# Kernel tuning notes

Hardware: AMD Instinct MI355X
Metric: run time of the kernel (lower is better)

The kernel has to match this reference:

```python
import jax, jax.numpy as jnp
import numpy as np

N, S, E, H = 2, 2048, 1024, 16
D = E // H  # head_dim = 64


def setup_inputs() -> dict:
    key = jax.random.key(0)
    k1, k2, k3 = jax.random.split(key, 3)
    x = jax.random.normal(k1, (N, S, E), dtype=jnp.float32)
    # Xavier-uniform-scaled weights (torch Linear layout: [out_features, in_features])
    lim_qkv = (6.0 / (E + 3 * E)) ** 0.5
    qkv_w = jax.random.uniform(k2, (3 * E, E), dtype=jnp.float32, minval=-lim_qkv, maxval=lim_qkv)
    lim_o = (6.0 / (E + E)) ** 0.5
    o_w = jax.random.uniform(k3, (E, E), dtype=jnp.float32, minval=-lim_o, maxval=lim_o)
    # causal look-ahead mask: positions where mask == 0 are excluded
    attn_mask = jnp.tril(jnp.ones((S, S), dtype=jnp.int32))
    return {"x": x, "attn_mask": attn_mask, "qkv_w": qkv_w, "o_w": o_w}


def reference(x, attn_mask, qkv_w, o_w):
    n, s, e = x.shape
    qkv = x @ qkv_w.T                              # (N, S, 3E)
    q, k, v = jnp.split(qkv, 3, axis=-1)
    # (N, S, E) -> (N, H, S, D)
    def to_heads(t):
        return t.reshape(n, s, H, D).transpose(0, 2, 1, 3)
    q, k, v = to_heads(q), to_heads(k), to_heads(v)
    scale = 1.0 / jnp.sqrt(jnp.asarray(D, dtype=x.dtype))
    logits = jnp.einsum('bhqd,bhkd->bhqk', q, k) * scale   # (N, H, S, S)
    mask = attn_mask.reshape(1, 1, s, s)                    # expand_mask: 2D -> (1,1,S,S)
    logits = jnp.where(mask == 0, -jnp.inf, logits)
    attn_weights = jax.nn.softmax(logits, axis=-1)
    values = jnp.einsum('bhqk,bhkd->bhqd', attn_weights, v)  # (N, H, S, D)
    values = values.transpose(0, 2, 1, 3).reshape(n, s, e)
    o = values @ o_w.T
    return o
```

## Files before the change

### kernel.cpp

```cpp
#include <hip/hip_runtime.h>
#include <math.h>

typedef unsigned short u16;
typedef unsigned int uint;
typedef __attribute__((ext_vector_type(8))) short bf16x8;
typedef __attribute__((ext_vector_type(8))) _Float16 half8;
typedef __attribute__((ext_vector_type(4))) float floatx4;

__device__ __forceinline__ u16 f2bf(float f) {
  union { float f; uint u; } c; c.f = f;
  return (u16)((c.u + 0x7FFFu + ((c.u >> 16) & 1u)) >> 16);
}
__device__ __forceinline__ float bf2f(u16 h) {
  union { uint u; float f; } c; c.u = ((uint)h) << 16;
  return c.f;
}
__device__ __forceinline__ u16 h2u(_Float16 h) {
  union { _Float16 h; u16 u; } c; c.h = h;
  return c.u;
}

#if __has_builtin(__builtin_amdgcn_exp2f)
#define EX2 __builtin_amdgcn_exp2f
#else
#define EX2 exp2f
#endif

__device__ __forceinline__ void gl_lds16(const u16* g, u16* l) {
  __builtin_amdgcn_global_load_lds(
      (const __attribute__((address_space(1))) uint*)g,
      (__attribute__((address_space(3))) uint*)l, 16, 0, 0);
}

__device__ __forceinline__ void store_c(u16* p, float v) { *p = f2bf(v); }
__device__ __forceinline__ void store_c(float* p, float v) { *p = v; }

#define ROR16(x, n)                                                        \
  __builtin_bit_cast(float, __builtin_amdgcn_update_dpp(                   \
      __builtin_bit_cast(int, (x)), __builtin_bit_cast(int, (x)),          \
      0x120 + (n), 0xF, 0xF, false))
__device__ __forceinline__ float rsum16(float x) {
  x += ROR16(x, 8); x += ROR16(x, 4); x += ROR16(x, 2); x += ROR16(x, 1);
  return x;
}

__global__ __launch_bounds__(256) void cvt_all(const float* __restrict__ x,
                                               const float* __restrict__ qw,
                                               const float* __restrict__ ow,
                                               u16* __restrict__ xb,
                                               u16* __restrict__ wb,
                                               u16* __restrict__ ob) {
  int bx = blockIdx.x;
  const float* src; u16* dst; int off;
  if (bx < 2048) { src = x; dst = xb; off = bx; }
  else if (bx < 3584) { src = qw; dst = wb; off = bx - 2048; }
  else { src = ow; dst = ob; off = bx - 3584; }
  int i = (off * 256 + threadIdx.x) * 8;
  float4 a = *(const float4*)(src + i);
  float4 b = *(const float4*)(src + i + 4);
  bf16x8 r;
  r[0] = (short)f2bf(a.x); r[1] = (short)f2bf(a.y);
  r[2] = (short)f2bf(a.z); r[3] = (short)f2bf(a.w);
  r[4] = (short)f2bf(b.x); r[5] = (short)f2bf(b.y);
  r[6] = (short)f2bf(b.z); r[7] = (short)f2bf(b.w);
  *(bf16x8*)(dst + i) = r;
}

__global__ __launch_bounds__(256) void vtrans(const u16* __restrict__ qkv,
                                              u16* __restrict__ vt) {
  constexpr int S = 2048, E = 1024, TE = 3072;
  __shared__ u16 tile[64 * 72];
  const int t = threadIdx.x;
  const int kv0 = blockIdx.x * 64;
  const int bh = blockIdx.y, b = bh >> 4, h = bh & 15;
  const u16* src = qkv + (size_t)b * S * TE + 2 * E + h * 64;
#pragma unroll
  for (int i = 0; i < 2; ++i) {
    int c = t + i * 256;
    int kv = c >> 3, d0 = (c & 7) * 8;
    *(bf16x8*)&tile[kv * 72 + d0] = *(const bf16x8*)&src[(size_t)(kv0 + kv) * TE + d0];
  }
  __syncthreads();
  u16* dst = vt + (size_t)bh * 64 * S + kv0;
#pragma unroll
  for (int i = 0; i < 2; ++i) {
    int c = t + i * 256;
    int d = c >> 3, k0 = (c & 7) * 8;
    bf16x8 r;
#pragma unroll
    for (int j = 0; j < 8; ++j)
      r[j] = (short)h2u((_Float16)bf2f(tile[(k0 + j) * 72 + d]));
    *(bf16x8*)&dst[(size_t)d * S + k0] = r;
  }
}

template <typename TC>
__global__ __launch_bounds__(256) void gemm_bt(const u16* __restrict__ A,
                                               const u16* __restrict__ B,
                                               TC* __restrict__ C,
                                               int K, int N) {
  __shared__ __align__(16) u16 lds_a[128 * 64];
  __shared__ __align__(16) u16 lds_b[128 * 64];
  const int t = threadIdx.x;
  const int w = t >> 6, lane = t & 63, quad = lane >> 4, lr = lane & 15;
  const int wr = w >> 1, wc = w & 1;
  const int m0 = blockIdx.y * 128, n0 = blockIdx.x * 128;

  const int srow = lane >> 3;
  const int scol = ((lane & 7) ^ srow) * 8;
  const u16* Ab = A + (size_t)(m0 + w * 32 + srow) * K + scol;
  const u16* Bb = B + (size_t)(n0 + w * 32 + srow) * K + scol;
  u16* la = lds_a + (w * 32) * 64;
  u16* lb = lds_b + (w * 32) * 64;

  floatx4 acc[4][4];
#pragma unroll
  for (int i = 0; i < 4; ++i)
#pragma unroll
    for (int j = 0; j < 4; ++j) acc[i][j] = {0.f, 0.f, 0.f, 0.f};

  for (int k0 = 0; k0 < K; k0 += 64) {
#pragma unroll
    for (int j = 0; j < 4; ++j) {
      gl_lds16(Ab + (size_t)(j * 8) * K + k0, la + j * 8 * 64);
      gl_lds16(Bb + (size_t)(j * 8) * K + k0, lb + j * 8 * 64);
    }
    __syncthreads();
#pragma unroll
    for (int kk = 0; kk < 2; ++kk) {
      bf16x8 af[4], bfr[4];
#pragma unroll
      for (int mi = 0; mi < 4; ++mi)
        af[mi] = *(const bf16x8*)&lds_a[(wr * 64 + mi * 16 + lr) * 64 +
                                        (((kk * 4 + quad) ^ (lr & 7)) * 8)];
#pragma unroll
      for (int ni = 0; ni < 4; ++ni)
        bfr[ni] = *(const bf16x8*)&lds_b[(wc * 64 + ni * 16 + lr) * 64 +
                                         (((kk * 4 + quad) ^ (lr & 7)) * 8)];
#pragma unroll
      for (int mi = 0; mi < 4; ++mi)
#pragma unroll
        for (int ni = 0; ni < 4; ++ni)
          acc[mi][ni] = __builtin_amdgcn_mfma_f32_16x16x32_bf16(
              af[mi], bfr[ni], acc[mi][ni], 0, 0, 0);
    }
    __syncthreads();
  }
#pragma unroll
  for (int mi = 0; mi < 4; ++mi)
#pragma unroll
    for (int r = 0; r < 4; ++r) {
      int m = m0 + wr * 64 + mi * 16 + quad * 4 + r;
#pragma unroll
      for (int ni = 0; ni < 4; ++ni) {
        int n = n0 + wc * 64 + ni * 16 + lr;
        store_c(&C[(size_t)m * N + n], acc[mi][ni][r]);
      }
    }
}

__global__ __launch_bounds__(256) void attn_fwd(const u16* __restrict__ qkv,
                                                const u16* __restrict__ vt,
                                                u16* __restrict__ out) {
  constexpr int S = 2048, E = 1024, TE = 3072;
  constexpr float NEG = -1e30f;
  __shared__ __align__(16) u16 lds_k[2][128 * 64];
  __shared__ __align__(16) u16 lds_vt[2][64 * 128];
  __shared__ __align__(16) u16 lds_p[64 * 128];
  const int t = threadIdx.x;
  const int w = t >> 6, lane = t & 63, quad = lane >> 4, lr = lane & 15;
  const int lin = (int)blockIdx.x;
  const int xcd = lin & 7, j = lin >> 3;
  const int bh = xcd + 8 * (j & 3);
  const int bx = j >> 2;
  const int b = bh >> 4, h = bh & 15;
  const size_t base = (size_t)b * S * TE;
  const u16* kbase = qkv + base + E + h * 64;
  const u16* vtb = vt + (size_t)bh * 64 * S;

  const int srow = lane >> 3;
  const int scol = ((lane & 7) ^ srow) * 8;
  const int vrow = lane >> 4;

  for (int ph = 0; ph < 2; ++ph) {
    const int qt = ph ? (31 - bx) : bx;
    const int q0 = qt * 64;
    const int nkt = (qt + 2) >> 1;

    const float QS = 0.125f * 1.44269504f;
    bf16x8 qf[2];
#pragma unroll
    for (int kk = 0; kk < 2; ++kk) {
      bf16x8 q = *(const bf16x8*)&qkv[base + (size_t)(q0 + w * 16 + lr) * TE +
                                      h * 64 + kk * 32 + quad * 8];
#pragma unroll
      for (int jj = 0; jj < 8; ++jj) q[jj] = (short)f2bf(bf2f((u16)q[jj]) * QS);
      qf[kk] = q;
    }

    float lst[4];
    floatx4 oacc[4];
#pragma unroll
    for (int r = 0; r < 4; ++r) lst[r] = 0.f;
#pragma unroll
    for (int di = 0; di < 4; ++di) oacc[di] = {0.f, 0.f, 0.f, 0.f};

    __syncthreads();

#pragma unroll
    for (int i = 0; i < 4; ++i) {
      int r0 = w * 8 + i * 32;
      gl_lds16(kbase + (size_t)(r0 + srow) * TE + scol, &lds_k[0][r0 * 64]);
    }
#pragma unroll
    for (int i = 0; i < 4; ++i) {
      int d0 = w * 4 + i * 16;
      int d = d0 + vrow;
      int cbg = ((lane & 15) ^ (d & 15)) * 8;
      gl_lds16(vtb + (size_t)d * S + cbg, &lds_vt[0][d0 * 128]);
    }

    for (int kt = 0; kt < nkt; ++kt) {
      const int bi = kt & 1;
      __syncthreads();
      if (kt + 1 < nkt) {
        const int bn = bi ^ 1;
#pragma unroll
        for (int i = 0; i < 4; ++i) {
          int r0 = w * 8 + i * 32;
          gl_lds16(kbase + (size_t)(128 * (kt + 1) + r0 + srow) * TE + scol,
                   &lds_k[bn][r0 * 64]);
        }
#pragma unroll
        for (int i = 0; i < 4; ++i) {
          int d0 = w * 4 + i * 16;
          int d = d0 + vrow;
          int cbg = ((lane & 15) ^ (d & 15)) * 8;
          gl_lds16(vtb + (size_t)d * S + 128 * (kt + 1) + cbg,
                   &lds_vt[bn][d0 * 128]);
        }
      }

      floatx4 st[8];
#pragma unroll
      for (int ni = 0; ni < 8; ++ni) st[ni] = {-4.f, -4.f, -4.f, -4.f};
#pragma unroll
      for (int kk = 0; kk < 2; ++kk) {
        bf16x8 kb[8];
#pragma unroll
        for (int ni = 0; ni < 8; ++ni)
          kb[ni] = *(const bf16x8*)&lds_k[bi][(ni * 16 + lr) * 64 +
                                             (((kk * 4 + quad) ^ (lr & 7)) * 8)];
#pragma unroll
        for (int ni = 0; ni < 8; ++ni)
          st[ni] = __builtin_amdgcn_mfma_f32_16x16x32_bf16(qf[kk], kb[ni], st[ni], 0, 0, 0);
      }

      const bool diag = (kt == nkt - 1);
      const int doff = (qt & 1) ? 64 : 0;
#pragma unroll
      for (int r = 0; r < 4; ++r) {
        const int rl = w * 16 + quad * 4 + r;
        if (diag) {
          const int thr = rl + doff;
#pragma unroll
          for (int ni = 0; ni < 8; ++ni)
            if (ni * 16 + lr > thr) st[ni][r] = NEG;
        }
        float pv[8];
#pragma unroll
        for (int ni = 0; ni < 8; ++ni) pv[ni] = EX2(st[ni][r]);
        lst[r] += ((pv[0] + pv[1]) + (pv[2] + pv[3])) +
                  ((pv[4] + pv[5]) + (pv[6] + pv[7]));
        const int swr = rl & 15;
#pragma unroll
        for (int ni = 0; ni < 8; ++ni) {
          int cb = (ni << 1) + (lr >> 3);
          lds_p[rl * 128 + (((cb ^ swr) << 3) + (lr & 7))] = h2u((_Float16)pv[ni]);
        }
      }

#pragma unroll
      for (int kk = 0; kk < 4; ++kk) {
        const int rl2 = w * 16 + lr;
        half8 pf = *(const half8*)&lds_p[rl2 * 128 + ((((kk << 2) + quad) ^ lr) << 3)];
        half8 vb[4];
#pragma unroll
        for (int di = 0; di < 4; ++di)
          vb[di] = *(const half8*)&lds_vt[bi][(di * 16 + lr) * 128 +
                                              ((((kk << 2) + quad) ^ lr) << 3)];
#pragma unroll
        for (int di = 0; di < 4; ++di)
          oacc[di] = __builtin_amdgcn_mfma_f32_16x16x32_f16(pf, vb[di], oacc[di], 0, 0, 0);
      }
    }

#pragma unroll
    for (int r = 0; r < 4; ++r) {
      int sg = q0 + w * 16 + quad * 4 + r;
      float inv_l = 1.f / rsum16(lst[r]);
#pragma unroll
      for (int di = 0; di < 4; ++di)
        out[((size_t)(b * S + sg)) * E + h * 64 + di * 16 + lr] =
            f2bf(oacc[di][r] * inv_l);
    }
  }
}

extern "C" void kernel_launch(void* const* d_in, const int* in_sizes, int n_in,
                              void* d_out, int out_size, void* d_ws, size_t ws_size,
                              hipStream_t stream) {
  constexpr int NB = 2, S = 2048, E = 1024;
  constexpr int M = NB * S;
  const float* x = (const float*)d_in[0];
  const float* qkv_w = (const float*)d_in[2];
  const float* o_w = (const float*)d_in[3];
  float* out = (float*)d_out;

  u16* qkv = (u16*)d_ws;
  u16* vt = qkv + (size_t)M * 3 * E;
  u16* xb = vt + (size_t)32 * 64 * S;
  u16* attn_o = xb;
  u16* wb = xb + (size_t)M * E;
  u16* ob = wb + (size_t)3 * E * E;

  cvt_all<<<4096, 256, 0, stream>>>(x, qkv_w, o_w, xb, wb, ob);
  gemm_bt<u16><<<dim3(3 * E / 128, M / 128), 256, 0, stream>>>(xb, wb, qkv, E, 3 * E);
  vtrans<<<dim3(S / 64, NB * 16), 256, 0, stream>>>(qkv, vt);
  attn_fwd<<<512, 256, 0, stream>>>(qkv, vt, attn_o);
  gemm_bt<float><<<dim3(E / 128, M / 128), 256, 0, stream>>>(attn_o, ob, out, E, E);
}
```

Before: 187.5 us.

## Enlarge attention query tile to 128 rows and add 64-row output GEMM

Attention blocks now each process 128 query rows, with each wave handling two 16-row groups, so every K/V tile loaded into shared memory is reused twice as much. K rows are loaded in a permuted order so that each lane's S values land contiguously, which lets the P tile be written to a per-wave buffer with vector stores. V fragments are hoisted out of the row-group loop. The grid is halved to 256 blocks with launch_bounds(256,1). The output projection switches to a 64x128-tile GEMM that launches more blocks. Register pressure grows and the grid may underfill the CUs.

```diff
diff --git a/kernel.cpp b/kernel.cpp
--- a/kernel.cpp
+++ b/kernel.cpp
@@ -159,58 +159,129 @@
     }
 }
 
-__global__ __launch_bounds__(256) void attn_fwd(const u16* __restrict__ qkv,
-                                                const u16* __restrict__ vt,
-                                                u16* __restrict__ out) {
+template <typename TC>
+__global__ __launch_bounds__(256) void gemm_bt64(const u16* __restrict__ A,
+                                                 const u16* __restrict__ B,
+                                                 TC* __restrict__ C,
+                                                 int K, int N) {
+  __shared__ __align__(16) u16 lds_a[64 * 64];
+  __shared__ __align__(16) u16 lds_b[128 * 64];
+  const int t = threadIdx.x;
+  const int w = t >> 6, lane = t & 63, quad = lane >> 4, lr = lane & 15;
+  const int m0 = blockIdx.y * 64, n0 = blockIdx.x * 128;
+
+  const int srow = lane >> 3;
+  const int scol = ((lane & 7) ^ srow) * 8;
+  const u16* Ab = A + (size_t)(m0 + srow) * K + scol;
+  const u16* Bb = B + (size_t)(n0 + srow) * K + scol;
+
+  floatx4 acc[4][2];
+#pragma unroll
+  for (int i = 0; i < 4; ++i)
+#pragma unroll
+    for (int j = 0; j < 2; ++j) acc[i][j] = {0.f, 0.f, 0.f, 0.f};
+
+  for (int k0 = 0; k0 < K; k0 += 64) {
+#pragma unroll
+    for (int i = 0; i < 2; ++i)
+      gl_lds16(Ab + (size_t)((w * 2 + i) * 8) * K + k0, &lds_a[(w * 2 + i) * 8 * 64]);
+#pragma unroll
+    for (int i = 0; i < 4; ++i)
+      gl_lds16(Bb + (size_t)((w * 4 + i) * 8) * K + k0, &lds_b[(w * 4 + i) * 8 * 64]);
+    __syncthreads();
+#pragma unroll
+    for (int kk = 0; kk < 2; ++kk) {
+      bf16x8 af[4], bfr[2];
+#pragma unroll
+      for (int mi = 0; mi < 4; ++mi)
+        af[mi] = *(const bf16x8*)&lds_a[(mi * 16 + lr) * 64 +
+                                        (((kk * 4 + quad) ^ (lr & 7)) * 8)];
+#pragma unroll
+      for (int ni = 0; ni < 2; ++ni)
+        bfr[ni] = *(const bf16x8*)&lds_b[(w * 32 + ni * 16 + lr) * 64 +
+                                         (((kk * 4 + quad) ^ (lr & 7)) * 8)];
+#pragma unroll
+      for (int mi = 0; mi < 4; ++mi)
+#pragma unroll
+        for (int ni = 0; ni < 2; ++ni)
+          acc[mi][ni] = __builtin_amdgcn_mfma_f32_16x16x32_bf16(
+              af[mi], bfr[ni], acc[mi][ni], 0, 0, 0);
+    }
+    __syncthreads();
+  }
+#pragma unroll
+  for (int mi = 0; mi < 4; ++mi)
+#pragma unroll
+    for (int r = 0; r < 4; ++r) {
+      int m = m0 + mi * 16 + quad * 4 + r;
+#pragma unroll
+      for (int ni = 0; ni < 2; ++ni) {
+        int n = n0 + w * 32 + ni * 16 + lr;
+        store_c(&C[(size_t)m * N + n], acc[mi][ni][r]);
+      }
+    }
+}
+
+__global__ __launch_bounds__(256, 1) void attn_fwd(const u16* __restrict__ qkv,
+                                                   const u16* __restrict__ vt,
+                                                   u16* __restrict__ out) {
   constexpr int S = 2048, E = 1024, TE = 3072;
   constexpr float NEG = -1e30f;
   __shared__ __align__(16) u16 lds_k[2][128 * 64];
   __shared__ __align__(16) u16 lds_vt[2][64 * 128];
-  __shared__ __align__(16) u16 lds_p[64 * 128];
+  __shared__ __align__(16) u16 lds_p[4][16 * 128];
   const int t = threadIdx.x;
   const int w = t >> 6, lane = t & 63, quad = lane >> 4, lr = lane & 15;
   const int lin = (int)blockIdx.x;
   const int xcd = lin & 7, j = lin >> 3;
   const int bh = xcd + 8 * (j & 3);
-  const int bx = j >> 2;
+  const int pr = j >> 2;
   const int b = bh >> 4, h = bh & 15;
   const size_t base = (size_t)b * S * TE;
   const u16* kbase = qkv + base + E + h * 64;
   const u16* vtb = vt + (size_t)bh * 64 * S;
 
-  const int srow = lane >> 3;
-  const int scol = ((lane & 7) ^ srow) * 8;
+  const int s8 = lane >> 3;
+  const int kcol = ((lane & 7) ^ s8) * 8;
   const int vrow = lane >> 4;
+  u16* const pb = &lds_p[w][0];
 
   for (int ph = 0; ph < 2; ++ph) {
-    const int qt = ph ? (31 - bx) : bx;
-    const int q0 = qt * 64;
-    const int nkt = (qt + 2) >> 1;
+    const int qt = ph ? (15 - pr) : pr;
+    const int q0 = qt * 128;
+    const int nkt = qt + 1;
 
     const float QS = 0.125f * 1.44269504f;
-    bf16x8 qf[2];
-#pragma unroll
-    for (int kk = 0; kk < 2; ++kk) {
-      bf16x8 q = *(const bf16x8*)&qkv[base + (size_t)(q0 + w * 16 + lr) * TE +
-                                      h * 64 + kk * 32 + quad * 8];
-#pragma unroll
-      for (int jj = 0; jj < 8; ++jj) q[jj] = (short)f2bf(bf2f((u16)q[jj]) * QS);
-      qf[kk] = q;
-    }
-
-    float lst[4];
-    floatx4 oacc[4];
-#pragma unroll
-    for (int r = 0; r < 4; ++r) lst[r] = 0.f;
-#pragma unroll
-    for (int di = 0; di < 4; ++di) oacc[di] = {0.f, 0.f, 0.f, 0.f};
+    bf16x8 qf[2][2];
+#pragma unroll
+    for (int rg = 0; rg < 2; ++rg)
+#pragma unroll
+      for (int kk = 0; kk < 2; ++kk) {
+        bf16x8 q = *(const bf16x8*)&qkv[base +
+            (size_t)(q0 + w * 32 + rg * 16 + lr) * TE + h * 64 + kk * 32 + quad * 8];
+#pragma unroll
+        for (int jj = 0; jj < 8; ++jj) q[jj] = (short)f2bf(bf2f((u16)q[jj]) * QS);
+        qf[rg][kk] = q;
+      }
+
+    float lst[2][4];
+    floatx4 oacc[2][4];
+#pragma unroll
+    for (int rg = 0; rg < 2; ++rg)
+#pragma unroll
+      for (int r = 0; r < 4; ++r) { lst[rg][r] = 0.f; }
+#pragma unroll
+    for (int rg = 0; rg < 2; ++rg)
+#pragma unroll
+      for (int di = 0; di < 4; ++di) oacc[rg][di] = {0.f, 0.f, 0.f, 0.f};
 
     __syncthreads();
 
 #pragma unroll
     for (int i = 0; i < 4; ++i) {
-      int r0 = w * 8 + i * 32;
-      gl_lds16(kbase + (size_t)(r0 + srow) * TE + scol, &lds_k[0][r0 * 64]);
+      int p0 = w * 8 + i * 32;
+      int kv = ((p0 & 15) + s8) * 8 + (p0 >> 4);
+      gl_lds16(kbase + (size_t)kv * TE + kcol, &lds_k[0][p0 * 64]);
     }
 #pragma unroll
     for (int i = 0; i < 4; ++i) {
@@ -227,9 +298,9 @@
         const int bn = bi ^ 1;
 #pragma unroll
         for (int i = 0; i < 4; ++i) {
-          int r0 = w * 8 + i * 32;
-          gl_lds16(kbase + (size_t)(128 * (kt + 1) + r0 + srow) * TE + scol,
-                   &lds_k[bn][r0 * 64]);
+          int p0 = w * 8 + i * 32;
+          int kv = 128 * (kt + 1) + ((p0 & 15) + s8) * 8 + (p0 >> 4);
+          gl_lds16(kbase + (size_t)kv * TE + kcol, &lds_k[bn][p0 * 64]);
         }
 #pragma unroll
         for (int i = 0; i < 4; ++i) {
@@ -241,9 +312,11 @@
         }
       }
 
-      floatx4 st[8];
-#pragma unroll
-      for (int ni = 0; ni < 8; ++ni) st[ni] = {-4.f, -4.f, -4.f, -4.f};
+      floatx4 st[2][8];
+#pragma unroll
+      for (int rg = 0; rg < 2; ++rg)
+#pragma unroll
+        for (int ni = 0; ni < 8; ++ni) st[rg][ni] = {-4.f, -4.f, -4.f, -4.f};
 #pragma unroll
       for (int kk = 0; kk < 2; ++kk) {
         bf16x8 kb[8];
@@ -252,58 +325,66 @@
           kb[ni] = *(const bf16x8*)&lds_k[bi][(ni * 16 + lr) * 64 +
                                              (((kk * 4 + quad) ^ (lr & 7)) * 8)];
 #pragma unroll
-        for (int ni = 0; ni < 8; ++ni)
-          st[ni] = __builtin_amdgcn_mfma_f32_16x16x32_bf16(qf[kk], kb[ni], st[ni], 0, 0, 0);
-      }
+        for (int rg = 0; rg < 2; ++rg)
+#pragma unroll
+          for (int ni = 0; ni < 8; ++ni)
+            st[rg][ni] = __builtin_amdgcn_mfma_f32_16x16x32_bf16(
+                qf[rg][kk], kb[ni], st[rg][ni], 0, 0, 0);
+      }
+
+      half8 vb[4][4];
+#pragma unroll
+      for (int kk = 0; kk < 4; ++kk)
+#pragma unroll
+        for (int di = 0; di < 4; ++di)
+          vb[kk][di] = *(const half8*)&lds_vt[bi][(di * 16 + lr) * 128 +
+                                                  (((kk * 4 + quad) ^ lr) << 3)];
 
       const bool diag = (kt == nkt - 1);
-      const int doff = (qt & 1) ? 64 : 0;
+#pragma unroll
+      for (int rg = 0; rg < 2; ++rg) {
+#pragma unroll
+        for (int r = 0; r < 4; ++r) {
+          const int rw = quad * 4 + r;
+          const int rloc = w * 32 + rg * 16 + rw;
+          if (diag) {
+#pragma unroll
+            for (int ni = 0; ni < 8; ++ni)
+              if (lr * 8 + ni > rloc) st[rg][ni][r] = NEG;
+          }
+          float pv[8];
+#pragma unroll
+          for (int ni = 0; ni < 8; ++ni) pv[ni] = EX2(st[rg][ni][r]);
+          lst[rg][r] += ((pv[0] + pv[1]) + (pv[2] + pv[3])) +
+                        ((pv[4] + pv[5]) + (pv[6] + pv[7]));
+          half8 p8;
+#pragma unroll
+          for (int ni = 0; ni < 8; ++ni) p8[ni] = (_Float16)pv[ni];
+          *(half8*)&pb[rw * 128 + (((lr + rw) & 15) << 3)] = p8;
+        }
+#pragma unroll
+        for (int kk = 0; kk < 4; ++kk) {
+          half8 pf = *(const half8*)&pb[lr * 128 +
+                                        ((((kk * 4 + quad) + lr) & 15) << 3)];
+#pragma unroll
+          for (int di = 0; di < 4; ++di)
+            oacc[rg][di] = __builtin_amdgcn_mfma_f32_16x16x32_f16(
+                pf, vb[kk][di], oacc[rg][di], 0, 0, 0);
+        }
+      }
+    }
+
+#pragma unroll
+    for (int rg = 0; rg < 2; ++rg)
 #pragma unroll
       for (int r = 0; r < 4; ++r) {
-        const int rl = w * 16 + quad * 4 + r;
-        if (diag) {
-          const int thr = rl + doff;
-#pragma unroll
-          for (int ni = 0; ni < 8; ++ni)
-            if (ni * 16 + lr > thr) st[ni][r] = NEG;
-        }
-        float pv[8];
-#pragma unroll
-        for (int ni = 0; ni < 8; ++ni) pv[ni] = EX2(st[ni][r]);
-        lst[r] += ((pv[0] + pv[1]) + (pv[2] + pv[3])) +
-                  ((pv[4] + pv[5]) + (pv[6] + pv[7]));
-        const int swr = rl & 15;
-#pragma unroll
-        for (int ni = 0; ni < 8; ++ni) {
-          int cb = (ni << 1) + (lr >> 3);
-          lds_p[rl * 128 + (((cb ^ swr) << 3) + (lr & 7))] = h2u((_Float16)pv[ni]);
-        }
-      }
-
-#pragma unroll
-      for (int kk = 0; kk < 4; ++kk) {
-        const int rl2 = w * 16 + lr;
-        half8 pf = *(const half8*)&lds_p[rl2 * 128 + ((((kk << 2) + quad) ^ lr) << 3)];
-        half8 vb[4];
+        int sg = q0 + w * 32 + rg * 16 + quad * 4 + r;
+        float inv_l = 1.f / rsum16(lst[rg][r]);
 #pragma unroll
         for (int di = 0; di < 4; ++di)
-          vb[di] = *(const half8*)&lds_vt[bi][(di * 16 + lr) * 128 +
-                                              ((((kk << 2) + quad) ^ lr) << 3)];
-#pragma unroll
-        for (int di = 0; di < 4; ++di)
-          oacc[di] = __builtin_amdgcn_mfma_f32_16x16x32_f16(pf, vb[di], oacc[di], 0, 0, 0);
-      }
-    }
-
-#pragma unroll
-    for (int r = 0; r < 4; ++r) {
-      int sg = q0 + w * 16 + quad * 4 + r;
-      float inv_l = 1.f / rsum16(lst[r]);
-#pragma unroll
-      for (int di = 0; di < 4; ++di)
-        out[((size_t)(b * S + sg)) * E + h * 64 + di * 16 + lr] =
-            f2bf(oacc[di][r] * inv_l);
-    }
+          out[((size_t)(b * S + sg)) * E + h * 64 + di * 16 + lr] =
+              f2bf(oacc[rg][di][r] * inv_l);
+      }
   }
 }
 
@@ -327,6 +408,6 @@
   cvt_all<<<4096, 256, 0, stream>>>(x, qkv_w, o_w, xb, wb, ob);
   gemm_bt<u16><<<dim3(3 * E / 128, M / 128), 256, 0, stream>>>(xb, wb, qkv, E, 3 * E);
   vtrans<<<dim3(S / 64, NB * 16), 256, 0, stream>>>(qkv, vt);
-  attn_fwd<<<512, 256, 0, stream>>>(qkv, vt, attn_o);
-  gemm_bt<float><<<dim3(E / 128, M / 128), 256, 0, stream>>>(attn_o, ob, out, E, E);
-}
+  attn_fwd<<<256, 256, 0, stream>>>(qkv, vt, attn_o);
+  gemm_bt64<float><<<dim3(E / 128, M / 64), 256, 0, stream>>>(attn_o, ob, out, E, E);
+}
```

Result: no change. 187.4 us (-0.0%).
